# Kernel optimization log

Measured on AMD Instinct MI355X. Metric: run time of the kernel, lower is better.

## Reference

```python
import jax, jax.numpy as jnp
import numpy as np

BS, S1, S2, D_IN1, D_IN2, ATTN_DIM, HEADS = 4, 2048, 2048, 512, 512, 512, 8
HEAD_DIM = ATTN_DIM // HEADS
NEG = -1e23


def _layer_norm(x, g, b, eps=1e-5):
    m = jnp.mean(x, axis=-1, keepdims=True)
    v = jnp.mean((x - m) ** 2, axis=-1, keepdims=True)
    return (x - m) / jnp.sqrt(v + eps) * g + b


def setup_inputs() -> dict:
    key = jax.random.key(0)
    ks = jax.random.split(key, 12)
    s = 0.02
    return {
        "modal1": jax.random.normal(ks[0], (BS, S1, D_IN1), dtype=jnp.float32),
        "modal2": jax.random.normal(ks[1], (BS, S2, D_IN2), dtype=jnp.float32),
        "unpadding_mask1": jax.random.randint(ks[2], (BS, S1, 1), 0, 2, dtype=jnp.int32),
        "unpadding_mask2": jax.random.randint(ks[3], (BS, S2), 0, 2, dtype=jnp.int32),
        "Wq": jax.random.normal(ks[4], (D_IN1, ATTN_DIM), dtype=jnp.float32) * s,
        "bq": jnp.zeros((ATTN_DIM,), dtype=jnp.float32),
        "Wkv": jax.random.normal(ks[5], (D_IN2, ATTN_DIM), dtype=jnp.float32) * s,
        "bkv": jnp.zeros((ATTN_DIM,), dtype=jnp.float32),
        "ln1_g": jnp.ones((ATTN_DIM,), dtype=jnp.float32),
        "ln1_b": jnp.zeros((ATTN_DIM,), dtype=jnp.float32),
        "W1": jax.random.normal(ks[6], (ATTN_DIM, ATTN_DIM), dtype=jnp.float32) * s,
        "b1": jnp.zeros((ATTN_DIM,), dtype=jnp.float32),
        "W2": jax.random.normal(ks[7], (ATTN_DIM, ATTN_DIM), dtype=jnp.float32) * s,
        "b2": jnp.zeros((ATTN_DIM,), dtype=jnp.float32),
        "ln2_g": jnp.ones((ATTN_DIM,), dtype=jnp.float32),
        "ln2_b": jnp.zeros((ATTN_DIM,), dtype=jnp.float32),
    }


def reference(modal1, modal2, unpadding_mask1, unpadding_mask2,
              Wq, bq, Wkv, bkv, ln1_g, ln1_b, W1, b1, W2, b2, ln2_g, ln2_b):
    bs = modal1.shape[0]
    q = modal1 @ Wq + bq                       # (bs, s1, D)
    kv = modal2 @ Wkv + bkv                    # (bs, s2, D)
    q = q.reshape(bs, -1, HEADS, HEAD_DIM).transpose(0, 2, 1, 3)    # (bs,h,s1,hd)
    k = kv.reshape(bs, -1, HEADS, HEAD_DIM).transpose(0, 2, 1, 3)   # (bs,h,s2,hd)
    v = k                                       # original reuses k as v (no v_proj)
    # padding mask: (bs,s1,1) x (bs,1,s2) -> (bs,s1,s2) > 0
    m1 = unpadding_mask1.astype(jnp.float32)            # (bs, s1, 1)
    m2 = unpadding_mask2.astype(jnp.float32)[:, None, :]  # (bs, 1, s2)
    attn_mask = (m1 @ m2) > 0                            # (bs, s1, s2)
    scale = 1.0 / (float(ATTN_DIM) ** 0.5)               # NOTE: attn_dim, not head_dim
    logits = jnp.einsum('bhqd,bhkd->bhqk', q, k) * scale
    logits = logits + jnp.where(attn_mask[:, None, :, :], 0.0, NEG)
    attn = jax.nn.softmax(logits, axis=-1)
    attn_res = jnp.einsum('bhqk,bhkd->bhqd', attn, v)
    attn_res = attn_res.transpose(0, 2, 1, 3).reshape(bs, -1, ATTN_DIM)
    # dropout in eval mode == identity
    x = attn_res + modal1
    x = _layer_norm(x, ln1_g, ln1_b)
    residual = x
    _ffn_out = jnp.tanh(x @ W1 + b1) @ W2 + b2  # computed then DISCARDED (original bug)
    x = attn_res + residual                      # x = dropout(attn_res) + residual
    x = _layer_norm(x, ln2_g, ln2_b)
    return x
```

## Files before the change

kernel.cpp:

```cpp
#include <hip/hip_runtime.h>
#include <hip/hip_bf16.h>

#define BSZ 4
#define S1v 2048
#define S2v 2048
#define DM 512
#define NH 8
#define HD 64
#define SCALE 0.044194173824159216f
#define L2E 1.4426950408889634f
#define SC_L2E (0.044194173824159216f * 1.4426950408889634f)
#define CBIAS 0.0028152f
#define NEGB (-1e30f)

typedef __bf16 bf16x8 __attribute__((ext_vector_type(8)));
typedef float f32x4 __attribute__((ext_vector_type(4)));

__device__ __forceinline__ unsigned short f2bf(float f) {
  union { float f; unsigned u; } v; v.f = f;
  unsigned r = v.u + 0x7FFFu + ((v.u >> 16) & 1u);
  return (unsigned short)(r >> 16);
}
__device__ __forceinline__ unsigned asu(float f) {
  union { float f; unsigned u; } v; v.f = f; return v.u;
}

__global__ __launch_bounds__(256)
void wtrans(const float* __restrict__ W, unsigned short* __restrict__ Wt) {
  __shared__ float tile[32][33];
  const int tx = threadIdx.x, ty = threadIdx.y;
  const int n0 = blockIdx.x * 32, k0 = blockIdx.y * 32;
#pragma unroll
  for (int i = 0; i < 32; i += 8)
    tile[ty + i][tx] = W[(size_t)(k0 + ty + i) * DM + n0 + tx];
  __syncthreads();
#pragma unroll
  for (int i = 0; i < 32; i += 8)
    Wt[(size_t)(n0 + ty + i) * DM + k0 + tx] = f2bf(tile[tx][ty + i]);
}

__global__ __launch_bounds__(256)
void proj_gemm(const float* __restrict__ X, const unsigned short* __restrict__ Wt,
               const float* __restrict__ bias, unsigned short* __restrict__ Y) {
  __shared__ unsigned short Xs[128][72];
  __shared__ unsigned short Ws[128][72];
  const int tid = threadIdx.x;
  const int wv = tid >> 6, lane = tid & 63;
  const int ln = lane & 15, qd = lane >> 4, q8 = qd * 8;
  const int wm = (wv >> 1) * 64, wn = (wv & 1) * 64;
  const int m0 = blockIdx.x * 128, n0 = blockIdx.y * 128;
  f32x4 acc[4][4] = {};
  for (int k0 = 0; k0 < DM; k0 += 64) {
    __syncthreads();
#pragma unroll
    for (int i = 0; i < 8; ++i) {
      int cid = tid + i * 256;
      int r = cid >> 4, c4 = (cid & 15) * 4;
      const float4 v = *(const float4*)(X + (size_t)(m0 + r) * DM + k0 + c4);
      ushort4 bv;
      bv.x = f2bf(v.x); bv.y = f2bf(v.y); bv.z = f2bf(v.z); bv.w = f2bf(v.w);
      *(ushort4*)&Xs[r][c4] = bv;
    }
#pragma unroll
    for (int i = 0; i < 4; ++i) {
      int cid = tid + i * 256;
      int r = cid >> 3, ch = (cid & 7) * 8;
      *(uint4*)&Ws[r][ch] = *(const uint4*)(Wt + (size_t)(n0 + r) * DM + k0 + ch);
    }
    __syncthreads();
#pragma unroll
    for (int kk = 0; kk < 2; ++kk) {
      bf16x8 aF[4], bF[4];
#pragma unroll
      for (int i = 0; i < 4; ++i)
        aF[i] = *(const bf16x8*)&Xs[wm + 16 * i + ln][kk * 32 + q8];
#pragma unroll
      for (int j = 0; j < 4; ++j)
        bF[j] = *(const bf16x8*)&Ws[wn + 16 * j + ln][kk * 32 + q8];
#pragma unroll
      for (int i = 0; i < 4; ++i)
#pragma unroll
        for (int j = 0; j < 4; ++j)
          acc[i][j] = __builtin_amdgcn_mfma_f32_16x16x32_bf16(aF[i], bF[j], acc[i][j], 0, 0, 0);
    }
  }
#pragma unroll
  for (int i = 0; i < 4; ++i)
#pragma unroll
    for (int j = 0; j < 4; ++j) {
      const int n = n0 + wn + 16 * j + ln;
      const float bb = bias[n];
#pragma unroll
      for (int r = 0; r < 4; ++r) {
        const int m = m0 + wm + 16 * i + qd * 4 + r;
        Y[(size_t)m * DM + n] = f2bf(acc[i][j][r] + bb);
      }
    }
}

__global__ __launch_bounds__(256)
void ktrans(const unsigned short* __restrict__ K, unsigned short* __restrict__ Kt) {
  __shared__ unsigned short T[128][72];
  const int tid = threadIdx.x;
  const int bh = blockIdx.y, b = bh >> 3, h = bh & 7;
  const int s0 = blockIdx.x * 128;
#pragma unroll
  for (int i = 0; i < 4; ++i) {
    int cid = tid + i * 256;
    int r = cid >> 3, ch = (cid & 7) * 8;
    *(uint4*)&T[r][ch] =
        *(const uint4*)(K + (size_t)(b * S2v + s0 + r) * DM + h * HD + ch);
  }
  __syncthreads();
#pragma unroll
  for (int i = 0; i < 4; ++i) {
    int cid = tid + i * 256;
    int d = cid >> 4, a = cid & 15;
    ushort4 v0, v1;
    v0.x = T[16 * 0 + a][d]; v0.y = T[16 * 1 + a][d];
    v0.z = T[16 * 2 + a][d]; v0.w = T[16 * 3 + a][d];
    v1.x = T[16 * 4 + a][d]; v1.y = T[16 * 5 + a][d];
    v1.z = T[16 * 6 + a][d]; v1.w = T[16 * 7 + a][d];
    unsigned short* o = Kt + ((size_t)(bh * HD + d)) * (size_t)S2v + s0 + a * 8;
    *(ushort4*)o = v0;
    *(ushort4*)(o + 4) = v1;
  }
}

__global__ __launch_bounds__(256, 2)
void flash_attn(const unsigned short* __restrict__ Qb, const unsigned short* __restrict__ Kb,
                const unsigned short* __restrict__ Kt, const int* __restrict__ m1,
                const int* __restrict__ m2, float* __restrict__ attn) {
  __shared__ unsigned short Ks[128][72];
  __shared__ unsigned short Vts[64][136];
  __shared__ unsigned short Ps[4][32][136];
  __shared__ int m2s[128];

  const int tid = threadIdx.x;
  const int wv = tid >> 6, lane = tid & 63;
  const int ln = lane & 15, qd = lane >> 4, q8 = qd * 8;
  const int lin = blockIdx.x + (blockIdx.y << 4);
  const int lid = ((lin & 7) << 6) | (lin >> 3);
  const int bh = lid >> 4;
  const int b = bh >> 3, h = bh & 7;
  const int q0 = (lid & 15) << 7;

  bf16x8 aQ[2][2];
#pragma unroll
  for (int t = 0; t < 2; ++t) {
    const size_t rbase =
        ((size_t)(b * S1v + q0 + wv * 32 + t * 16 + ln)) * DM + h * HD;
    aQ[t][0] = *(const bf16x8*)(Qb + rbase + q8);
    aQ[t][1] = *(const bf16x8*)(Qb + rbase + 32 + q8);
  }

  float acoef[2][4];
#pragma unroll
  for (int t = 0; t < 2; ++t)
#pragma unroll
    for (int r = 0; r < 4; ++r)
      acoef[t][r] = (m1[b * S1v + q0 + wv * 32 + t * 16 + qd * 4 + r] == 0) ? 0.f : 1.f;

  float lrow[2][4] = {};
  f32x4 O[2][4] = {};

  for (int s0 = 0; s0 < S2v; s0 += 128) {
    __syncthreads();
#pragma unroll
    for (int i = 0; i < 4; ++i) {
      int cid = tid + i * 256;
      int r = cid >> 3, ch = (cid & 7) * 8;
      *(uint4*)&Ks[r][ch] =
          *(const uint4*)(Kb + ((size_t)(b * S2v + s0 + r)) * DM + h * HD + ch);
    }
#pragma unroll
    for (int i = 0; i < 4; ++i) {
      int cid = tid + i * 256;
      int r = cid >> 4, ch = (cid & 15) * 8;
      *(uint4*)&Vts[r][ch] =
          *(const uint4*)(Kt + ((size_t)(bh * HD + r)) * (size_t)S2v + s0 + ch);
    }
    if (tid < 128) m2s[tid] = m2[b * S2v + s0 + tid];
    __syncthreads();

    f32x4 sc[2][8];
#pragma unroll
    for (int j = 0; j < 8; ++j) {
      const bf16x8 b0 = *(const bf16x8*)&Ks[16 * j + ln][q8];
      const bf16x8 b1 = *(const bf16x8*)&Ks[16 * j + ln][32 + q8];
#pragma unroll
      for (int t = 0; t < 2; ++t) {
        f32x4 z = {};
        z = __builtin_amdgcn_mfma_f32_16x16x32_bf16(aQ[t][0], b0, z, 0, 0, 0);
        sc[t][j] = __builtin_amdgcn_mfma_f32_16x16x32_bf16(aQ[t][1], b1, z, 0, 0, 0);
      }
    }

    float moff[8];
#pragma unroll
    for (int j = 0; j < 8; ++j)
      moff[j] = (m2s[16 * j + ln] != 0) ? 0.f : NEGB;

#pragma unroll
    for (int t = 0; t < 2; ++t)
#pragma unroll
      for (int j = 0; j < 8; ++j)
#pragma unroll
        for (int r = 0; r < 4; ++r) {
          const float e = fmaf(acoef[t][r], fmaf(sc[t][j][r], SC_L2E, moff[j]), CBIAS);
          const float p = __builtin_amdgcn_exp2f(e);
          lrow[t][r] += p;
          sc[t][j][r] = p;
        }

#pragma unroll
    for (int t = 0; t < 2; ++t)
#pragma unroll
      for (int r = 0; r < 4; ++r) {
        uint4 dw;
        dw.x = __builtin_amdgcn_perm(asu(sc[t][1][r]), asu(sc[t][0][r]), 0x07060302u);
        dw.y = __builtin_amdgcn_perm(asu(sc[t][3][r]), asu(sc[t][2][r]), 0x07060302u);
        dw.z = __builtin_amdgcn_perm(asu(sc[t][5][r]), asu(sc[t][4][r]), 0x07060302u);
        dw.w = __builtin_amdgcn_perm(asu(sc[t][7][r]), asu(sc[t][6][r]), 0x07060302u);
        *(uint4*)&Ps[wv][t * 16 + qd * 4 + r][ln * 8] = dw;
      }
    __asm__ volatile("s_waitcnt lgkmcnt(0)" ::: "memory");

#pragma unroll
    for (int kk = 0; kk < 4; ++kk) {
      const bf16x8 aP0 = *(const bf16x8*)&Ps[wv][ln][kk * 32 + q8];
      const bf16x8 aP1 = *(const bf16x8*)&Ps[wv][16 + ln][kk * 32 + q8];
#pragma unroll
      for (int jn = 0; jn < 4; ++jn) {
        const bf16x8 bV = *(const bf16x8*)&Vts[16 * jn + ln][kk * 32 + q8];
        O[0][jn] = __builtin_amdgcn_mfma_f32_16x16x32_bf16(aP0, bV, O[0][jn], 0, 0, 0);
        O[1][jn] = __builtin_amdgcn_mfma_f32_16x16x32_bf16(aP1, bV, O[1][jn], 0, 0, 0);
      }
    }
  }

#pragma unroll
  for (int t = 0; t < 2; ++t)
#pragma unroll
    for (int r = 0; r < 4; ++r) {
      float l = lrow[t][r];
#pragma unroll
      for (int msk = 1; msk < 16; msk <<= 1) l += __shfl_xor(l, msk, 64);
      const float inv = l > 0.f ? 1.0f / l : 0.f;
      const int m = q0 + wv * 32 + t * 16 + qd * 4 + r;
#pragma unroll
      for (int jn = 0; jn < 4; ++jn)
        attn[((size_t)(b * S1v + m)) * DM + h * HD + 16 * jn + ln] = O[t][jn][r] * inv;
    }
}

__global__ __launch_bounds__(128)
void ln_fused(const float* __restrict__ attn, const float* __restrict__ modal1,
              const float* __restrict__ g1, const float* __restrict__ b1,
              const float* __restrict__ g2, const float* __restrict__ b2,
              float* __restrict__ out) {
  __shared__ float red[4];
  const int row = blockIdx.x, t = threadIdx.x;
  const size_t base = (size_t)row * DM + t * 4;
  const float4 a = *(const float4*)(attn + base);
  const float4 mo = *(const float4*)(modal1 + base);
  float av[4] = { a.x, a.y, a.z, a.w };
  float x[4] = { a.x + mo.x, a.y + mo.y, a.z + mo.z, a.w + mo.w };
  float s = 0.f, q = 0.f;
#pragma unroll
  for (int i = 0; i < 4; ++i) { s += x[i]; q += x[i] * x[i]; }
#pragma unroll
  for (int m = 1; m < 64; m <<= 1) { s += __shfl_xor(s, m, 64); q += __shfl_xor(q, m, 64); }
  if ((t & 63) == 0) { red[t >> 6] = s; red[2 + (t >> 6)] = q; }
  __syncthreads();
  s = red[0] + red[1]; q = red[2] + red[3];
  const float mu = s * (1.0f / DM);
  const float rinv = rsqrtf(q * (1.0f / DM) - mu * mu + 1e-5f);
  const int c = t * 4;
  const float4 G1 = *(const float4*)(g1 + c), B1 = *(const float4*)(b1 + c);
  const float gg1[4] = { G1.x, G1.y, G1.z, G1.w }, bb1[4] = { B1.x, B1.y, B1.z, B1.w };
  float y[4];
  float s2 = 0.f, q2 = 0.f;
#pragma unroll
  for (int i = 0; i < 4; ++i) {
    y[i] = av[i] + (x[i] - mu) * rinv * gg1[i] + bb1[i];
    s2 += y[i]; q2 += y[i] * y[i];
  }
#pragma unroll
  for (int m = 1; m < 64; m <<= 1) { s2 += __shfl_xor(s2, m, 64); q2 += __shfl_xor(q2, m, 64); }
  __syncthreads();
  if ((t & 63) == 0) { red[t >> 6] = s2; red[2 + (t >> 6)] = q2; }
  __syncthreads();
  s2 = red[0] + red[1]; q2 = red[2] + red[3];
  const float mu2 = s2 * (1.0f / DM);
  const float rinv2 = rsqrtf(q2 * (1.0f / DM) - mu2 * mu2 + 1e-5f);
  const float4 G2 = *(const float4*)(g2 + c), B2 = *(const float4*)(b2 + c);
  float4 o;
  o.x = (y[0] - mu2) * rinv2 * G2.x + B2.x;
  o.y = (y[1] - mu2) * rinv2 * G2.y + B2.y;
  o.z = (y[2] - mu2) * rinv2 * G2.z + B2.z;
  o.w = (y[3] - mu2) * rinv2 * G2.w + B2.w;
  *(float4*)(out + base) = o;
}

extern "C" void kernel_launch(void* const* d_in, const int* in_sizes, int n_in,
                              void* d_out, int out_size, void* d_ws, size_t ws_size,
                              hipStream_t stream) {
  const float* modal1 = (const float*)d_in[0];
  const float* modal2 = (const float*)d_in[1];
  const int*   m1     = (const int*)d_in[2];
  const int*   m2     = (const int*)d_in[3];
  const float* Wq     = (const float*)d_in[4];
  const float* bq     = (const float*)d_in[5];
  const float* Wkv    = (const float*)d_in[6];
  const float* bkv    = (const float*)d_in[7];
  const float* g1     = (const float*)d_in[8];
  const float* b1     = (const float*)d_in[9];
  const float* g2     = (const float*)d_in[14];
  const float* b2     = (const float*)d_in[15];
  float* out = (float*)d_out;

  char* ws = (char*)d_ws;
  unsigned short* q_bf  = (unsigned short*)(ws);
  unsigned short* k_bf  = (unsigned short*)(ws + 8388608);
  unsigned short* kt_bf = (unsigned short*)(ws + 16777216);
  unsigned short* wqt   = (unsigned short*)(ws + 25165824);
  unsigned short* wkt   = (unsigned short*)(ws + 25690112);
  float*          attn  = (float*)(ws + 26214400);

  dim3 tb(32, 8);
  wtrans<<<dim3(16, 16), tb, 0, stream>>>(Wq, wqt);
  wtrans<<<dim3(16, 16), tb, 0, stream>>>(Wkv, wkt);
  proj_gemm<<<dim3(64, 4), 256, 0, stream>>>(modal1, wqt, bq, q_bf);
  proj_gemm<<<dim3(64, 4), 256, 0, stream>>>(modal2, wkt, bkv, k_bf);
  ktrans<<<dim3(16, 32), 256, 0, stream>>>(k_bf, kt_bf);
  flash_attn<<<dim3(16, 32), 256, 0, stream>>>(q_bf, k_bf, kt_bf, m1, m2, attn);
  ln_fused<<<dim3(8192), 128, 0, stream>>>(attn, modal1, g1, b1, g2, b2, out);
}
```

Before: 203.2 us.

## Keep P in registers by swapping MFMA operands and permuting V transpose layout

Swaps the QK^T MFMA operand order so each lane holds scores for one query row across key columns, letting the bf16 probabilities be packed directly into MFMA A-operands. This removes the per-wave Ps shared-memory round trip and its wait. The K-transpose kernel permutes key order to match the new register layout of P. Mask handling is simplified to one row coefficient per lane and precomputed float key offsets in LDS. Occupancy hint rises to 3 blocks/SM, which may cause register spills.

New measurement: 201.5 us. No clear change (-0.8%).

```diff
diff --git a/kernel.cpp b/kernel.cpp
--- a/kernel.cpp
+++ b/kernel.cpp
@@ -116,25 +116,25 @@
   for (int i = 0; i < 4; ++i) {
     int cid = tid + i * 256;
     int d = cid >> 4, a = cid & 15;
+    const int base = 16 * (a >> 2) + 4 * (a & 3);
     ushort4 v0, v1;
-    v0.x = T[16 * 0 + a][d]; v0.y = T[16 * 1 + a][d];
-    v0.z = T[16 * 2 + a][d]; v0.w = T[16 * 3 + a][d];
-    v1.x = T[16 * 4 + a][d]; v1.y = T[16 * 5 + a][d];
-    v1.z = T[16 * 6 + a][d]; v1.w = T[16 * 7 + a][d];
+    v0.x = T[base + 0][d]; v0.y = T[base + 1][d];
+    v0.z = T[base + 2][d]; v0.w = T[base + 3][d];
+    v1.x = T[base + 64][d]; v1.y = T[base + 65][d];
+    v1.z = T[base + 66][d]; v1.w = T[base + 67][d];
     unsigned short* o = Kt + ((size_t)(bh * HD + d)) * (size_t)S2v + s0 + a * 8;
     *(ushort4*)o = v0;
     *(ushort4*)(o + 4) = v1;
   }
 }
 
-__global__ __launch_bounds__(256, 2)
+__global__ __launch_bounds__(256, 3)
 void flash_attn(const unsigned short* __restrict__ Qb, const unsigned short* __restrict__ Kb,
                 const unsigned short* __restrict__ Kt, const int* __restrict__ m1,
                 const int* __restrict__ m2, float* __restrict__ attn) {
   __shared__ unsigned short Ks[128][72];
   __shared__ unsigned short Vts[64][136];
-  __shared__ unsigned short Ps[4][32][136];
-  __shared__ int m2s[128];
+  __shared__ float m2f[128];
 
   const int tid = threadIdx.x;
   const int wv = tid >> 6, lane = tid & 63;
@@ -154,14 +154,12 @@
     aQ[t][1] = *(const bf16x8*)(Qb + rbase + 32 + q8);
   }
 
-  float acoef[2][4];
+  float acoef[2];
 #pragma unroll
   for (int t = 0; t < 2; ++t)
-#pragma unroll
-    for (int r = 0; r < 4; ++r)
-      acoef[t][r] = (m1[b * S1v + q0 + wv * 32 + t * 16 + qd * 4 + r] == 0) ? 0.f : 1.f;
-
-  float lrow[2][4] = {};
+    acoef[t] = (m1[b * S1v + q0 + wv * 32 + t * 16 + ln] == 0) ? 0.f : 1.f;
+
+  float lrow[2] = {};
   f32x4 O[2][4] = {};
 
   for (int s0 = 0; s0 < S2v; s0 += 128) {
@@ -180,77 +178,74 @@
       *(uint4*)&Vts[r][ch] =
           *(const uint4*)(Kt + ((size_t)(bh * HD + r)) * (size_t)S2v + s0 + ch);
     }
-    if (tid < 128) m2s[tid] = m2[b * S2v + s0 + tid];
+    if (tid < 128) m2f[tid] = (m2[b * S2v + s0 + tid] != 0) ? 0.f : NEGB;
     __syncthreads();
 
     f32x4 sc[2][8];
 #pragma unroll
     for (int j = 0; j < 8; ++j) {
-      const bf16x8 b0 = *(const bf16x8*)&Ks[16 * j + ln][q8];
-      const bf16x8 b1 = *(const bf16x8*)&Ks[16 * j + ln][32 + q8];
+      const bf16x8 k0f = *(const bf16x8*)&Ks[16 * j + ln][q8];
+      const bf16x8 k1f = *(const bf16x8*)&Ks[16 * j + ln][32 + q8];
 #pragma unroll
       for (int t = 0; t < 2; ++t) {
         f32x4 z = {};
-        z = __builtin_amdgcn_mfma_f32_16x16x32_bf16(aQ[t][0], b0, z, 0, 0, 0);
-        sc[t][j] = __builtin_amdgcn_mfma_f32_16x16x32_bf16(aQ[t][1], b1, z, 0, 0, 0);
+        z = __builtin_amdgcn_mfma_f32_16x16x32_bf16(k0f, aQ[t][0], z, 0, 0, 0);
+        sc[t][j] = __builtin_amdgcn_mfma_f32_16x16x32_bf16(k1f, aQ[t][1], z, 0, 0, 0);
       }
     }
 
-    float moff[8];
-#pragma unroll
-    for (int j = 0; j < 8; ++j)
-      moff[j] = (m2s[16 * j + ln] != 0) ? 0.f : NEGB;
-
-#pragma unroll
-    for (int t = 0; t < 2; ++t)
-#pragma unroll
-      for (int j = 0; j < 8; ++j)
+#pragma unroll
+    for (int j = 0; j < 8; ++j) {
+      const f32x4 mv = *(const f32x4*)&m2f[16 * j + 4 * qd];
+#pragma unroll
+      for (int t = 0; t < 2; ++t)
 #pragma unroll
         for (int r = 0; r < 4; ++r) {
-          const float e = fmaf(acoef[t][r], fmaf(sc[t][j][r], SC_L2E, moff[j]), CBIAS);
+          const float e = fmaf(acoef[t], fmaf(sc[t][j][r], SC_L2E, mv[r]), CBIAS);
           const float p = __builtin_amdgcn_exp2f(e);
-          lrow[t][r] += p;
+          lrow[t] += p;
           sc[t][j][r] = p;
         }
-
-#pragma unroll
-    for (int t = 0; t < 2; ++t)
-#pragma unroll
-      for (int r = 0; r < 4; ++r) {
-        uint4 dw;
-        dw.x = __builtin_amdgcn_perm(asu(sc[t][1][r]), asu(sc[t][0][r]), 0x07060302u);
-        dw.y = __builtin_amdgcn_perm(asu(sc[t][3][r]), asu(sc[t][2][r]), 0x07060302u);
-        dw.z = __builtin_amdgcn_perm(asu(sc[t][5][r]), asu(sc[t][4][r]), 0x07060302u);
-        dw.w = __builtin_amdgcn_perm(asu(sc[t][7][r]), asu(sc[t][6][r]), 0x07060302u);
-        *(uint4*)&Ps[wv][t * 16 + qd * 4 + r][ln * 8] = dw;
+    }
+
+#pragma unroll
+    for (int kk = 0; kk < 4; ++kk) {
+      bf16x8 aP[2];
+#pragma unroll
+      for (int t = 0; t < 2; ++t) {
+        union { uint4 u; bf16x8 v; } cvt;
+        cvt.u.x = __builtin_amdgcn_perm(asu(sc[t][kk][1]),     asu(sc[t][kk][0]),     0x07060302u);
+        cvt.u.y = __builtin_amdgcn_perm(asu(sc[t][kk][3]),     asu(sc[t][kk][2]),     0x07060302u);
+        cvt.u.z = __builtin_amdgcn_perm(asu(sc[t][kk + 4][1]), asu(sc[t][kk + 4][0]), 0x07060302u);
+        cvt.u.w = __builtin_amdgcn_perm(asu(sc[t][kk + 4][3]), asu(sc[t][kk + 4][2]), 0x07060302u);
+        aP[t] = cvt.v;
       }
-    __asm__ volatile("s_waitcnt lgkmcnt(0)" ::: "memory");
-
-#pragma unroll
-    for (int kk = 0; kk < 4; ++kk) {
-      const bf16x8 aP0 = *(const bf16x8*)&Ps[wv][ln][kk * 32 + q8];
-      const bf16x8 aP1 = *(const bf16x8*)&Ps[wv][16 + ln][kk * 32 + q8];
 #pragma unroll
       for (int jn = 0; jn < 4; ++jn) {
         const bf16x8 bV = *(const bf16x8*)&Vts[16 * jn + ln][kk * 32 + q8];
-        O[0][jn] = __builtin_amdgcn_mfma_f32_16x16x32_bf16(aP0, bV, O[0][jn], 0, 0, 0);
-        O[1][jn] = __builtin_amdgcn_mfma_f32_16x16x32_bf16(aP1, bV, O[1][jn], 0, 0, 0);
+        O[0][jn] = __builtin_amdgcn_mfma_f32_16x16x32_bf16(aP[0], bV, O[0][jn], 0, 0, 0);
+        O[1][jn] = __builtin_amdgcn_mfma_f32_16x16x32_bf16(aP[1], bV, O[1][jn], 0, 0, 0);
       }
     }
   }
 
+  float inv[2];
+#pragma unroll
+  for (int t = 0; t < 2; ++t) {
+    float l = lrow[t];
+    l += __shfl_xor(l, 16, 64);
+    l += __shfl_xor(l, 32, 64);
+    inv[t] = l > 0.f ? 1.0f / l : 0.f;
+  }
 #pragma unroll
   for (int t = 0; t < 2; ++t)
 #pragma unroll
     for (int r = 0; r < 4; ++r) {
-      float l = lrow[t][r];
-#pragma unroll
-      for (int msk = 1; msk < 16; msk <<= 1) l += __shfl_xor(l, msk, 64);
-      const float inv = l > 0.f ? 1.0f / l : 0.f;
+      const float invr = __shfl(inv[t], 4 * qd + r, 64);
       const int m = q0 + wv * 32 + t * 16 + qd * 4 + r;
 #pragma unroll
       for (int jn = 0; jn < 4; ++jn)
-        attn[((size_t)(b * S1v + m)) * DM + h * HD + 16 * jn + ln] = O[t][jn][r] * inv;
+        attn[((size_t)(b * S1v + m)) * DM + h * HD + 16 * jn + ln] = O[t][jn][r] * invr;
     }
 }
 
```
